# Performance work log

Hardware: AMD Instinct MI355X
Metric: run time of the kernel (lower is better)

Reference implementation:

```python
import jax, jax.numpy as jnp
import numpy as np

B, F, V, D, ND = 16384, 26, 100000, 64, 13
H1, H2, H3 = 1024, 512, 256


def setup_inputs() -> dict:
    key = jax.random.key(0)
    ks = jax.random.split(key, 12)
    s = 0.02
    return {
        "dense": jax.random.normal(ks[0], (B, ND), jnp.float32),
        "sparse_idx": jax.random.randint(ks[1], (B, F), 0, V),
        "bias": jnp.zeros((1, 1), jnp.float32),
        "emb_tables": jax.random.normal(ks[2], (F, V, D), jnp.float32) * s,
        "lin_tables": jax.random.normal(ks[3], (F, V), jnp.float32) * s,
        "Wd": jax.random.normal(ks[4], (ND, D), jnp.float32) * s,
        "Wld": jax.random.normal(ks[5], (ND, 1), jnp.float32) * s,
        "bld": jnp.zeros((1,), jnp.float32),
        "W1": jax.random.normal(ks[6], ((F + 1) * D, H1), jnp.float32) * s,
        "W2": jax.random.normal(ks[7], (H1, H2), jnp.float32) * s,
        "W3": jax.random.normal(ks[8], (H2, H3), jnp.float32) * s,
        "Wout": jax.random.normal(ks[9], (H3, 1), jnp.float32) * s,
    }


def reference(dense, sparse_idx, bias, emb_tables, lin_tables, Wd, Wld, bld, W1, W2, W3, Wout):
    feat = jnp.arange(F)[None, :]                      # [1,F] broadcasts with idx [B,F]
    sparse_emb = emb_tables[feat, sparse_idx]          # [B,F,D] batched multi-table gather
    dense_emb = dense @ Wd                             # [B,D]
    emb = jnp.concatenate([dense_emb[:, None, :], sparse_emb], axis=1)  # [B,F+1,D]

    # first-order term: linear dense + per-feature 1-dim embeddings
    first = dense @ Wld + bld + lin_tables[feat, sparse_idx].sum(axis=1, keepdims=True)  # [B,1]

    # FM second-order: 0.5 * sum_d ((sum_f e)^2 - sum_f e^2)
    sum_e = emb.sum(axis=1)                            # [B,D]
    second = 0.5 * (sum_e * sum_e - (emb * emb).sum(axis=1)).sum(axis=1, keepdims=True)  # [B,1]

    # deep part (dropout p=0 -> identity)
    h = emb.reshape(emb.shape[0], -1)                  # [B,(F+1)*D]
    h = jax.nn.relu(h @ W1)
    h = jax.nn.relu(h @ W2)
    h = jax.nn.relu(h @ W3)
    deep = h @ Wout                                    # [B,1]

    return bias + first + second + deep
```

## Files before the change

kernel.cpp:

```cpp
#include <hip/hip_runtime.h>
#include <hip/hip_bf16.h>

#define B_SAMP 16384
#define NFEAT 26
#define VOCAB 100000
#define DIM 64
#define NDENSE 13
#define H1 1024
#define H2 512
#define H3 256
#define KIN ((NFEAT + 1) * DIM)
#define KP1 1792

typedef int   i32x4 __attribute__((ext_vector_type(4)));
typedef int   i32x8 __attribute__((ext_vector_type(8)));
typedef float f32x4 __attribute__((ext_vector_type(4)));

__device__ inline void async_load16(const void* g, void* lds) {
  __builtin_amdgcn_global_load_lds(
      (const __attribute__((address_space(1))) void*)g,
      (__attribute__((address_space(3))) void*)lds, 16, 0, 0);
}

__device__ inline unsigned char f32_to_fp8(float v) {
  return (unsigned char)(__builtin_amdgcn_cvt_pk_fp8_f32(v, v, 0, false) & 0xff);
}

__global__ __launch_bounds__(256) void k_embed_fm(
    const float* __restrict__ dense, const int* __restrict__ sidx,
    const float* __restrict__ emb, const float* __restrict__ lin,
    const float* __restrict__ Wd, const float* __restrict__ Wld,
    const float* __restrict__ bld, const float* __restrict__ bias,
    unsigned char* __restrict__ h, float* __restrict__ out)
{
  int wave = threadIdx.x >> 6, lane = threadIdx.x & 63;
  int b = blockIdx.x * 4 + wave;
  const float* drow = dense + b * NDENSE;

  float de = 0.f;
#pragma unroll
  for (int nd = 0; nd < NDENSE; ++nd) de += drow[nd] * Wd[nd * DIM + lane];

  unsigned char* hrow = h + (size_t)b * KP1;
  hrow[lane] = f32_to_fp8(de);
  hrow[KIN + lane] = 0;
  float sum_e = de, sumsq = de * de;

  float fo = 0.f;
  if (lane < NDENSE) fo = drow[lane] * Wld[lane];

  const int* irow = sidx + b * NFEAT;
#pragma unroll
  for (int f = 0; f < NFEAT; ++f) {
    int ix = irow[f];
    float e = emb[((size_t)f * VOCAB + ix) * DIM + lane];
    sum_e += e; sumsq += e * e;
    hrow[(f + 1) * DIM + lane] = f32_to_fp8(e);
  }
  if (lane < NFEAT) fo += lin[(size_t)lane * VOCAB + irow[lane]];

  float sec = sum_e * sum_e - sumsq;
#pragma unroll
  for (int o = 32; o > 0; o >>= 1) {
    sec += __shfl_down(sec, o);
    fo  += __shfl_down(fo, o);
  }
  if (lane == 0) out[b] = fo + bld[0] + 0.5f * sec + bias[0];
}

__global__ __launch_bounds__(256) void k_prep_weights(
    const float* __restrict__ W1, const float* __restrict__ W2,
    const float* __restrict__ W3,
    unsigned char* __restrict__ W1t, unsigned char* __restrict__ W2t,
    unsigned char* __restrict__ W3t)
{
  __shared__ float tile[32][33];
  int id = blockIdx.x;
  const float* src; unsigned char* dst; int R, C, Rp, bx, by;
  if (id < 1792)      { src = W1; dst = W1t; R = KIN; C = H1; Rp = KP1; bx = id % 32; by = id / 32; }
  else if (id < 2304) { id -= 1792; src = W2; dst = W2t; R = H1; C = H2; Rp = H1; bx = id % 16; by = id / 16; }
  else                { id -= 2304; src = W3; dst = W3t; R = H2; C = H3; Rp = H2; bx = id % 8;  by = id / 8;  }
  int c0 = bx * 32, r0 = by * 32;
  int tx = threadIdx.x & 31, ty = threadIdx.x >> 5;
#pragma unroll
  for (int i = 0; i < 32; i += 8) {
    int r = r0 + ty + i;
    tile[ty + i][tx] = (r < R) ? src[(size_t)r * C + c0 + tx] : 0.f;
  }
  __syncthreads();
#pragma unroll
  for (int i = 0; i < 32; i += 8)
    dst[(size_t)(c0 + ty + i) * Rp + r0 + tx] = f32_to_fp8(tile[tx][ty + i]);
}

template <bool RELU, bool FP8OUT, bool REDUCE>
__global__ __launch_bounds__(256) void k_gemm_fp8(
    const unsigned char* __restrict__ A,
    const unsigned char* __restrict__ Bt,
    void* __restrict__ Cv, int M, int N, int K,
    const float* __restrict__ wo, float* __restrict__ outp)
{
  __shared__ unsigned char As[16384];
  __shared__ unsigned char Bs[16384];
  int tid = threadIdx.x;
  int wave = tid >> 6, lane = tid & 63;
  int wm = wave & 1, wn = wave >> 1;

  int gx = gridDim.x, gy = gridDim.y;
  int wg = blockIdx.y * gx + blockIdx.x;
  int cpx = (gx * gy) >> 3;
  int swz = (wg & 7) * cpx + (wg >> 3);
  int bm = (swz / gy) * 128, bn = (swz % gy) * 128;

  int l15 = lane & 15, quad = lane >> 4;

  f32x4 acc[4][4];
#pragma unroll
  for (int i = 0; i < 4; ++i)
#pragma unroll
    for (int j = 0; j < 4; ++j) acc[i][j] = (f32x4){0.f, 0.f, 0.f, 0.f};

  int nk = K >> 7;
  for (int kt = 0; kt < nk; ++kt) {
    int k0 = kt << 7;
    __syncthreads();
#pragma unroll
    for (int s = 0; s < 2; ++s) {
      int st = 2 * wave + s;
      size_t ga = (size_t)(bm + st * 16 + l15) * K + k0 + quad * 32;
      size_t gb = (size_t)(bn + st * 16 + l15) * K + k0 + quad * 32;
#pragma unroll
      for (int j = 0; j < 2; ++j) {
        async_load16(A + ga + j * 16, &As[st * 2048 + j * 1024]);
        async_load16(Bt + gb + j * 16, &Bs[st * 2048 + j * 1024]);
      }
    }
    __syncthreads();

    i32x8 af[4], bf[4];
#pragma unroll
    for (int i = 0; i < 4; ++i) {
      {
        i32x4 lo = *(const i32x4*)&As[(4 * wm + i) * 2048 + lane * 16];
        i32x4 hi = *(const i32x4*)&As[(4 * wm + i) * 2048 + 1024 + lane * 16];
        af[i] = (i32x8){lo.x, lo.y, lo.z, lo.w, hi.x, hi.y, hi.z, hi.w};
      }
      {
        i32x4 lo = *(const i32x4*)&Bs[(4 * wn + i) * 2048 + lane * 16];
        i32x4 hi = *(const i32x4*)&Bs[(4 * wn + i) * 2048 + 1024 + lane * 16];
        bf[i] = (i32x8){lo.x, lo.y, lo.z, lo.w, hi.x, hi.y, hi.z, hi.w};
      }
    }
#pragma unroll
    for (int mi = 0; mi < 4; ++mi)
#pragma unroll
      for (int ni = 0; ni < 4; ++ni)
        acc[mi][ni] = __builtin_amdgcn_mfma_scale_f32_16x16x128_f8f6f4(
            af[mi], bf[ni], acc[mi][ni],
            0 , 0 , 0, 0x7f7f7f7f, 0, 0x7f7f7f7f);
  }

  if (REDUCE) {
    float wv[4];
#pragma unroll
    for (int ni = 0; ni < 4; ++ni) wv[ni] = wo[bn + 64 * wn + 16 * ni + l15];
#pragma unroll
    for (int mi = 0; mi < 4; ++mi)
#pragma unroll
      for (int r = 0; r < 4; ++r) {
        float s = 0.f;
#pragma unroll
        for (int ni = 0; ni < 4; ++ni)
          s += fmaxf(acc[mi][ni][r], 0.f) * wv[ni];
        s += __shfl_xor(s, 1);
        s += __shfl_xor(s, 2);
        s += __shfl_xor(s, 4);
        s += __shfl_xor(s, 8);
        if (l15 == 0)
          atomicAdd(outp + bm + 64 * wm + 16 * mi + quad * 4 + r, s);
      }
  } else {
#pragma unroll
    for (int mi = 0; mi < 4; ++mi)
#pragma unroll
      for (int ni = 0; ni < 4; ++ni)
#pragma unroll
        for (int r = 0; r < 4; ++r) {
          int m = bm + 64 * wm + 16 * mi + quad * 4 + r;
          int n = bn + 64 * wn + 16 * ni + l15;
          float v = acc[mi][ni][r];
          if (RELU) v = fmaxf(v, 0.f);
          if (FP8OUT) ((unsigned char*)Cv)[(size_t)m * N + n] = f32_to_fp8(v);
          else        ((float*)Cv)[(size_t)m * N + n] = v;
        }
  }
}

extern "C" void kernel_launch(void* const* d_in, const int* in_sizes, int n_in,
                              void* d_out, int out_size, void* d_ws, size_t ws_size,
                              hipStream_t stream) {
  const float* dense = (const float*)d_in[0];
  const int*   sidx  = (const int*)d_in[1];
  const float* bias  = (const float*)d_in[2];
  const float* emb   = (const float*)d_in[3];
  const float* lin   = (const float*)d_in[4];
  const float* Wd    = (const float*)d_in[5];
  const float* Wld   = (const float*)d_in[6];
  const float* bld   = (const float*)d_in[7];
  const float* W1    = (const float*)d_in[8];
  const float* W2    = (const float*)d_in[9];
  const float* W3    = (const float*)d_in[10];
  const float* Wout  = (const float*)d_in[11];
  float* out = (float*)d_out;

  char* ws = (char*)d_ws;
  const size_t o_h   = 0;
  const size_t o_a1  = 29360128;
  const size_t o_a2  = 46137344;
  const size_t o_w1t = 54525952;
  const size_t o_w2t = 56360960;
  const size_t o_w3t = 56885248;

  unsigned char* h   = (unsigned char*)(ws + o_h);
  unsigned char* a1  = (unsigned char*)(ws + o_a1);
  unsigned char* a2  = (unsigned char*)(ws + o_a2);
  unsigned char* W1t = (unsigned char*)(ws + o_w1t);
  unsigned char* W2t = (unsigned char*)(ws + o_w2t);
  unsigned char* W3t = (unsigned char*)(ws + o_w3t);

  k_prep_weights<<<2432, 256, 0, stream>>>(W1, W2, W3, W1t, W2t, W3t);

  k_embed_fm<<<B_SAMP / 4, 256, 0, stream>>>(dense, sidx, emb, lin, Wd, Wld, bld,
                                             bias, h, out);

  k_gemm_fp8<true, true,  false><<<dim3(B_SAMP / 128, H1 / 128), 256, 0, stream>>>(
      h,  W1t, a1, B_SAMP, H1, KP1, nullptr, nullptr);
  k_gemm_fp8<true, true,  false><<<dim3(B_SAMP / 128, H2 / 128), 256, 0, stream>>>(
      a1, W2t, a2, B_SAMP, H2, H1, nullptr, nullptr);
  k_gemm_fp8<true, false, true ><<<dim3(B_SAMP / 128, H3 / 128), 256, 0, stream>>>(
      a2, W3t, nullptr, B_SAMP, H3, H2, Wout, out);
}
```

Before: 851.0 us.

## Merge weight prep into embed kernel and vectorize embedding gather with packed fp8 stores

The separate weight-transpose kernel is folded into the embedding/FM kernel as extra blocks, so one launch does both and the two jobs can overlap on the GPU. Inside the embedding path, each lane now loads a float4 slice and a wave covers four features per iteration, replacing one-float-per-lane gathers and per-byte fp8 stores with 16-byte loads and packed 4-byte fp8 stores. The FM second-order term is recomputed through cross-group shuffles, with a 0.25 factor to correct for the total being replicated across the four feature groups. This adds shuffle work and a more complex kernel with mixed block roles.

```diff
diff --git a/kernel.cpp b/kernel.cpp
--- a/kernel.cpp
+++ b/kernel.cpp
@@ -26,71 +26,103 @@
   return (unsigned char)(__builtin_amdgcn_cvt_pk_fp8_f32(v, v, 0, false) & 0xff);
 }
 
-__global__ __launch_bounds__(256) void k_embed_fm(
+__device__ inline unsigned int pack_fp8x4(float a, float b, float c, float d) {
+  unsigned int r = __builtin_amdgcn_cvt_pk_fp8_f32(a, b, 0u, false);
+  r = __builtin_amdgcn_cvt_pk_fp8_f32(c, d, r, true);
+  return r;
+}
+
+__global__ __launch_bounds__(256) void k_embed_prep(
     const float* __restrict__ dense, const int* __restrict__ sidx,
     const float* __restrict__ emb, const float* __restrict__ lin,
     const float* __restrict__ Wd, const float* __restrict__ Wld,
     const float* __restrict__ bld, const float* __restrict__ bias,
-    unsigned char* __restrict__ h, float* __restrict__ out)
-{
-  int wave = threadIdx.x >> 6, lane = threadIdx.x & 63;
-  int b = blockIdx.x * 4 + wave;
-  const float* drow = dense + b * NDENSE;
-
-  float de = 0.f;
-#pragma unroll
-  for (int nd = 0; nd < NDENSE; ++nd) de += drow[nd] * Wd[nd * DIM + lane];
-
-  unsigned char* hrow = h + (size_t)b * KP1;
-  hrow[lane] = f32_to_fp8(de);
-  hrow[KIN + lane] = 0;
-  float sum_e = de, sumsq = de * de;
-
-  float fo = 0.f;
-  if (lane < NDENSE) fo = drow[lane] * Wld[lane];
-
-  const int* irow = sidx + b * NFEAT;
-#pragma unroll
-  for (int f = 0; f < NFEAT; ++f) {
-    int ix = irow[f];
-    float e = emb[((size_t)f * VOCAB + ix) * DIM + lane];
-    sum_e += e; sumsq += e * e;
-    hrow[(f + 1) * DIM + lane] = f32_to_fp8(e);
-  }
-  if (lane < NFEAT) fo += lin[(size_t)lane * VOCAB + irow[lane]];
-
-  float sec = sum_e * sum_e - sumsq;
-#pragma unroll
-  for (int o = 32; o > 0; o >>= 1) {
-    sec += __shfl_down(sec, o);
-    fo  += __shfl_down(fo, o);
-  }
-  if (lane == 0) out[b] = fo + bld[0] + 0.5f * sec + bias[0];
-}
-
-__global__ __launch_bounds__(256) void k_prep_weights(
+    unsigned char* __restrict__ h, float* __restrict__ out,
     const float* __restrict__ W1, const float* __restrict__ W2,
     const float* __restrict__ W3,
     unsigned char* __restrict__ W1t, unsigned char* __restrict__ W2t,
     unsigned char* __restrict__ W3t)
 {
   __shared__ float tile[32][33];
-  int id = blockIdx.x;
-  const float* src; unsigned char* dst; int R, C, Rp, bx, by;
-  if (id < 1792)      { src = W1; dst = W1t; R = KIN; C = H1; Rp = KP1; bx = id % 32; by = id / 32; }
-  else if (id < 2304) { id -= 1792; src = W2; dst = W2t; R = H1; C = H2; Rp = H1; bx = id % 16; by = id / 16; }
-  else                { id -= 2304; src = W3; dst = W3t; R = H2; C = H3; Rp = H2; bx = id % 8;  by = id / 8;  }
-  int c0 = bx * 32, r0 = by * 32;
-  int tx = threadIdx.x & 31, ty = threadIdx.x >> 5;
-#pragma unroll
-  for (int i = 0; i < 32; i += 8) {
-    int r = r0 + ty + i;
-    tile[ty + i][tx] = (r < R) ? src[(size_t)r * C + c0 + tx] : 0.f;
-  }
-  __syncthreads();
-#pragma unroll
-  for (int i = 0; i < 32; i += 8)
-    dst[(size_t)(c0 + ty + i) * Rp + r0 + tx] = f32_to_fp8(tile[tx][ty + i]);
+
+  if (blockIdx.x >= 4096) {
+    int id = blockIdx.x - 4096;
+    const float* src; unsigned char* dst; int R, C, Rp, bx, by;
+    if (id < 1792)      { src = W1; dst = W1t; R = KIN; C = H1; Rp = KP1; bx = id % 32; by = id / 32; }
+    else if (id < 2304) { id -= 1792; src = W2; dst = W2t; R = H1; C = H2; Rp = H1; bx = id % 16; by = id / 16; }
+    else                { id -= 2304; src = W3; dst = W3t; R = H2; C = H3; Rp = H2; bx = id % 8;  by = id / 8;  }
+    int c0 = bx * 32, r0 = by * 32;
+    int tx = threadIdx.x & 31, ty = threadIdx.x >> 5;
+#pragma unroll
+    for (int i = 0; i < 32; i += 8) {
+      int r = r0 + ty + i;
+      tile[ty + i][tx] = (r < R) ? src[(size_t)r * C + c0 + tx] : 0.f;
+    }
+    __syncthreads();
+#pragma unroll
+    for (int i = 0; i < 32; i += 8)
+      dst[(size_t)(c0 + ty + i) * Rp + r0 + tx] = f32_to_fp8(tile[tx][ty + i]);
+    return;
+  }
+
+  int wave = threadIdx.x >> 6, lane = threadIdx.x & 63;
+  int b = blockIdx.x * 4 + wave;
+  const float* drow = dense + b * NDENSE;
+  const int*   irow = sidx + b * NFEAT;
+  int fg = lane >> 4;
+  int dq = lane & 15;
+
+  int myidx = (lane < NFEAT) ? irow[lane] : 0;
+
+  float dx = 0.f, dy = 0.f, dz = 0.f, dw = 0.f;
+#pragma unroll
+  for (int nd = 0; nd < NDENSE; ++nd) {
+    float dv = drow[nd];
+    const f32x4 w = *(const f32x4*)&Wd[nd * DIM + 4 * dq];
+    dx += dv * w.x; dy += dv * w.y; dz += dv * w.z; dw += dv * w.w;
+  }
+
+  unsigned char* hrow = h + (size_t)b * KP1;
+  float Sx, Sy, Sz, Sw, q;
+  if (fg == 0) {
+    Sx = dx; Sy = dy; Sz = dz; Sw = dw;
+    q = dx * dx + dy * dy + dz * dz + dw * dw;
+    *(unsigned int*)&hrow[4 * dq] = pack_fp8x4(dx, dy, dz, dw);
+  } else {
+    Sx = Sy = Sz = Sw = 0.f; q = 0.f;
+  }
+  if (fg == 1) *(unsigned int*)&hrow[KIN + 4 * dq] = 0u;
+
+  float fo = 0.f;
+  if (lane < NDENSE) fo = drow[lane] * Wld[lane];
+  if (lane < NFEAT)  fo += lin[(size_t)lane * VOCAB + myidx];
+
+#pragma unroll
+  for (int g = 0; g < 7; ++g) {
+    int f = 4 * g + fg;
+    int ix = __shfl(myidx, f & 31);
+    if (f < NFEAT) {
+      const f32x4 e = *(const f32x4*)(emb + ((size_t)f * VOCAB + ix) * DIM + 4 * dq);
+      Sx += e.x; Sy += e.y; Sz += e.z; Sw += e.w;
+      q += e.x * e.x + e.y * e.y + e.z * e.z + e.w * e.w;
+      *(unsigned int*)&hrow[(f + 1) * DIM + 4 * dq] = pack_fp8x4(e.x, e.y, e.z, e.w);
+    }
+  }
+
+#pragma unroll
+  for (int off = 16; off < 64; off <<= 1) {
+    Sx += __shfl_xor(Sx, off);
+    Sy += __shfl_xor(Sy, off);
+    Sz += __shfl_xor(Sz, off);
+    Sw += __shfl_xor(Sw, off);
+  }
+  float u = 0.25f * (Sx * Sx + Sy * Sy + Sz * Sz + Sw * Sw) - q;
+#pragma unroll
+  for (int o = 32; o > 0; o >>= 1) {
+    u  += __shfl_down(u, o);
+    fo += __shfl_down(fo, o);
+  }
+  if (lane == 0) out[b] = fo + bld[0] + 0.5f * u + bias[0];
 }
 
 template <bool RELU, bool FP8OUT, bool REDUCE>
@@ -228,10 +260,9 @@
   unsigned char* W2t = (unsigned char*)(ws + o_w2t);
   unsigned char* W3t = (unsigned char*)(ws + o_w3t);
 
-  k_prep_weights<<<2432, 256, 0, stream>>>(W1, W2, W3, W1t, W2t, W3t);
-
-  k_embed_fm<<<B_SAMP / 4, 256, 0, stream>>>(dense, sidx, emb, lin, Wd, Wld, bld,
-                                             bias, h, out);
+  k_embed_prep<<<4096 + 2432, 256, 0, stream>>>(
+      dense, sidx, emb, lin, Wd, Wld, bld, bias, h, out,
+      W1, W2, W3, W1t, W2t, W3t);
 
   k_gemm_fp8<true, true,  false><<<dim3(B_SAMP / 128, H1 / 128), 256, 0, stream>>>(
       h,  W1t, a1, B_SAMP, H1, KP1, nullptr, nullptr);
```

Measured after the change: 848.0 us. No clear change (-0.3%).
